# Kernel tuning notes

Hardware: AMD Instinct MI355X
Metric: run time of the kernel (lower is better)

Reference implementation:

```python
import jax, jax.numpy as jnp
import numpy as np

TEMP = 10.0
BPE = 4
BER = 0.01
K = 2 ** BPE  # number of centers


def setup_inputs() -> dict:
    key = jax.random.key(0)
    k1, k2 = jax.random.split(key)
    x = jax.random.normal(k1, (32, 256, 32, 32), dtype=jnp.float32)
    center = jax.random.normal(k2, (K,), dtype=jnp.float32)
    return {"x": x, "center": center}


def reference(x, center):
    # Q_type == 'Soft' path of quantizer_channel.forward
    # residuals to every center: [B, C, H, W, K]
    d = x[..., None] - center
    # nearest-center index (hard assignment)
    W_index = jnp.argmin(jnp.abs(d), axis=-1)  # int32 [B,C,H,W]
    # soft assignment and soft quantized value
    smx = jax.nn.softmax(-TEMP * (d * d), axis=-1)
    W_soft = jnp.einsum('bchwk,k->bchw', smx, center)
    # bitmap rows are the binary expansion of the index, MSB first;
    # map[W_index][..., j] == (W_index >> (BPE-1-j)) & 1
    shifts = jnp.arange(BPE - 1, -1, -1, dtype=jnp.int32)  # [BPE]
    bits = (W_index[..., None] >> shifts) & 1  # [B,C,H,W,BPE]
    # bernoulli bit-flip channel noise; (bit + noise) % 2 == XOR
    noise = jax.random.bernoulli(jax.random.key(42), BER, bits.shape).astype(bits.dtype)
    noisy_bits = bits ^ noise
    # index = sum_i 2^i * bits[..., BPE-1-i]  ==  dot with 2^shifts
    idx_noisy = jnp.sum(noisy_bits * (2 ** shifts), axis=-1)
    W_noisy = center[idx_noisy]
    # soft value with stop-gradient channel bias (straight-through noise)
    return W_soft + jax.lax.stop_gradient(W_noisy - W_soft)
```

## Files before the change

kernel.cpp:

```cpp
#include <hip/hip_runtime.h>
#include <stdint.h>


#define KS1 42u
#define KS2 0x1BD11BF0u
#define BERN_LT 42950144u

__device__ __forceinline__ uint32_t fkey(float f) {
  uint32_t u = __float_as_uint(f);
  return (u & 0x80000000u) ? ~u : (u | 0x80000000u);
}
__device__ __forceinline__ float finv(uint32_t k) {
  uint32_t u = (k & 0x80000000u) ? (k & 0x7fffffffu) : ~k;
  return __uint_as_float(u);
}

__global__ void quantizer_setup_kernel(const float* __restrict__ center,
                                       float* __restrict__ ws) {
  const int t = threadIdx.x;
  __shared__ float sval[16];
  __shared__ int   sidx[16];
  if (t < 16) {
    const float ct = center[t];
    int rank = 0;
    for (int j = 0; j < 16; ++j) {
      const float cj = center[j];
      rank += (cj < ct || (cj == ct && j < t)) ? 1 : 0;
    }
    sval[rank] = ct;
    sidx[rank] = t;
  }
  __syncthreads();
  if (t < 15) {
    const float sL = sval[t], sR = sval[t + 1];
    const bool tieLeft = sidx[t] < sidx[t + 1];
    uint32_t lo = fkey(sL), hi = fkey(sR);
    while (hi - lo > 1u) {
      const uint32_t mid = lo + ((hi - lo) >> 1);
      const float xm = finv(mid);
      const float dL = fabsf(xm - sL);
      const float dR = fabsf(xm - sR);
      const bool left = (dL < dR) || (dL == dR && tieLeft);
      if (left) lo = mid; else hi = mid;
    }
    ws[t] = finv(lo);
  }
  __syncthreads();
  if (t < 16) {
    ((uint32_t*)ws)[16 + t] = (uint32_t)sidx[t];
    if (t == 15) ((uint32_t*)ws)[15] = 0u;
  }
}

__device__ __forceinline__ uint32_t rotl(uint32_t x, int r) {
  return __builtin_amdgcn_alignbit(x, x, (32 - r) & 31);
}
#define TF_ROUND4(r)                                            \
  { _Pragma("unroll") for (int j = 0; j < 4; ++j) {             \
      y0[j] += y1[j];                                           \
      y1[j] = rotl(y1[j], (r)) ^ y0[j];                         \
  } }
#define TF_INJ4(a, b)                                           \
  { _Pragma("unroll") for (int j = 0; j < 4; ++j) {             \
      y0[j] += (a); y1[j] += (b);                               \
  } }

__global__ __launch_bounds__(256) void quantizer_channel_kernel(
    const float* __restrict__ x, const float* __restrict__ center,
    const float* __restrict__ ws, float* __restrict__ out, int n4)
{
  const int t = blockIdx.x * blockDim.x + threadIdx.x;
  if (t >= n4) return;

  const int lane   = threadIdx.x & 63;
  const int base_b = (lane & 48) << 2;

  const int ctab = __float_as_int(center[lane & 15]);
  const int stab = (int)((const uint32_t*)ws)[16 + (lane & 15)];

  const float4* wsf = (const float4*)ws;
  const float4 ta = wsf[0], tb = wsf[1], tc = wsf[2], td = wsf[3];
  const float T0 = ta.x, T1 = ta.y, T2  = ta.z, T3  = ta.w;
  const float T4 = tb.x, T5 = tb.y, T6  = tb.z, T7  = tb.w;
  const float T8 = tc.x, T9 = tc.y, T10 = tc.z, T11 = tc.w;
  const float T12 = td.x, T13 = td.y, T14 = td.z;

  const float4 xv = reinterpret_cast<const float4*>(x)[t];
  const float xe[4] = {xv.x, xv.y, xv.z, xv.w};
  float oe[4];
  const uint32_t cb = (uint32_t)t * 16u + KS1;

#pragma unroll
  for (int e = 0; e < 4; ++e) {
    uint32_t y0[4], y1[4];
    const uint32_t c0 = cb + 4u * (uint32_t)e;
#pragma unroll
    for (int j = 0; j < 4; ++j) { y0[j] = 0u; y1[j] = c0 + (uint32_t)j; }
    TF_ROUND4(13) TF_ROUND4(15) TF_ROUND4(26) TF_ROUND4(6)
    TF_INJ4(KS1, KS2 + 1u)
    TF_ROUND4(17) TF_ROUND4(29) TF_ROUND4(16) TF_ROUND4(24)
    TF_INJ4(KS2, 0u + 2u)
    TF_ROUND4(13) TF_ROUND4(15) TF_ROUND4(26) TF_ROUND4(6)
    TF_INJ4(0u, KS1 + 3u)
    TF_ROUND4(17) TF_ROUND4(29) TF_ROUND4(16) TF_ROUND4(24)
    TF_INJ4(KS1, KS2 + 4u)
    TF_ROUND4(13) TF_ROUND4(15) TF_ROUND4(26) TF_ROUND4(6)
    TF_INJ4(KS2, 0u + 5u)

    const uint32_t f =
        (((y0[0] ^ y1[0]) < BERN_LT) ? 8u : 0u) |
        (((y0[1] ^ y1[1]) < BERN_LT) ? 4u : 0u) |
        (((y0[2] ^ y1[2]) < BERN_LT) ? 2u : 0u) |
        (((y0[3] ^ y1[3]) < BERN_LT) ? 1u : 0u);

    const float v = xe[e];
    const bool b3_ = v > T7;
    const float s2 = b3_ ? T11 : T3;
    const bool b2_ = v > s2;
    const float s1 = b3_ ? (b2_ ? T13 : T9) : (b2_ ? T5 : T1);
    const bool b1_ = v > s1;
    const float u0 = b1_ ? T2  : T0;
    const float u1 = b1_ ? T6  : T4;
    const float u2 = b1_ ? T10 : T8;
    const float u3 = b1_ ? T14 : T12;
    const float s0 = b3_ ? (b2_ ? u3 : u2) : (b2_ ? u1 : u0);
    const bool b0_ = v > s0;
    const uint32_t cell = (b3_ ? 8u : 0u) | (b2_ ? 4u : 0u) |
                          (b1_ ? 2u : 0u) | (b0_ ? 1u : 0u);

    const int best = __builtin_amdgcn_ds_bpermute(base_b + (int)(cell << 2), stab);
    const int fin_addr = base_b + (int)((((uint32_t)best) ^ f) << 2);
    oe[e] = __int_as_float(__builtin_amdgcn_ds_bpermute(fin_addr, ctab));
  }

  float4 o4;
  o4.x = oe[0]; o4.y = oe[1]; o4.z = oe[2]; o4.w = oe[3];
  reinterpret_cast<float4*>(out)[t] = o4;
}

extern "C" void kernel_launch(void* const* d_in, const int* in_sizes, int n_in,
                              void* d_out, int out_size, void* d_ws, size_t ws_size,
                              hipStream_t stream)
{
  const float* x      = (const float*)d_in[0];
  const float* center = (const float*)d_in[1];
  float* out          = (float*)d_out;
  float* ws           = (float*)d_ws;

  hipLaunchKernelGGL(quantizer_setup_kernel, dim3(1), dim3(64), 0, stream,
                     center, ws);

  const int N  = in_sizes[0];
  const int n4 = N / 4;
  const int block = 256;
  const int grid  = (n4 + block - 1) / block;

  hipLaunchKernelGGL(quantizer_channel_kernel, dim3(grid), dim3(block), 0, stream,
                     x, center, ws, out, n4);
}
```

Baseline: 72.66 us.

## Split threefry noise generation into separate kernel with packed flip masks

Moves the Bernoulli noise generation (threefry hashing) into its own kernel, which writes one packed 16-bit flip mask per float4 into the workspace. A second kernel then does the centre lookup and the XOR using those stored masks. The intent is to separate the compute-heavy RNG from the memory-bound quantize pass so each kernel is simpler. In exchange it adds an extra kernel launch and extra global-memory traffic for writing and reading the masks. It falls back to the original fused kernel when the workspace is too small.

```diff
diff --git a/kernel.cpp b/kernel.cpp
--- a/kernel.cpp
+++ b/kernel.cpp
@@ -5,6 +5,7 @@
 #define KS1 42u
 #define KS2 0x1BD11BF0u
 #define BERN_LT 42950144u
+#define WS_FLIP_OFF 32
 
 __device__ __forceinline__ uint32_t fkey(float f) {
   uint32_t u = __float_as_uint(f);
@@ -64,10 +65,46 @@
   { _Pragma("unroll") for (int j = 0; j < 4; ++j) {             \
       y0[j] += (a); y1[j] += (b);                               \
   } }
-
-__global__ __launch_bounds__(256) void quantizer_channel_kernel(
+#define TF_BODY                                                 \
+  TF_ROUND4(13) TF_ROUND4(15) TF_ROUND4(26) TF_ROUND4(6)       \
+  TF_INJ4(KS1, KS2 + 1u)                                        \
+  TF_ROUND4(17) TF_ROUND4(29) TF_ROUND4(16) TF_ROUND4(24)      \
+  TF_INJ4(KS2, 0u + 2u)                                         \
+  TF_ROUND4(13) TF_ROUND4(15) TF_ROUND4(26) TF_ROUND4(6)       \
+  TF_INJ4(0u, KS1 + 3u)                                         \
+  TF_ROUND4(17) TF_ROUND4(29) TF_ROUND4(16) TF_ROUND4(24)      \
+  TF_INJ4(KS1, KS2 + 4u)                                        \
+  TF_ROUND4(13) TF_ROUND4(15) TF_ROUND4(26) TF_ROUND4(6)       \
+  TF_INJ4(KS2, 0u + 5u)
+
+__global__ __launch_bounds__(256) void noise_kernel(
+    uint16_t* __restrict__ flips, int n4)
+{
+  const int t = blockIdx.x * blockDim.x + threadIdx.x;
+  if (t >= n4) return;
+  const uint32_t cb = (uint32_t)t * 16u + KS1;
+  uint32_t packed = 0u;
+#pragma unroll
+  for (int e = 0; e < 4; ++e) {
+    uint32_t y0[4], y1[4];
+    const uint32_t c0 = cb + 4u * (uint32_t)e;
+#pragma unroll
+    for (int j = 0; j < 4; ++j) { y0[j] = 0u; y1[j] = c0 + (uint32_t)j; }
+    TF_BODY
+    const uint32_t nib =
+        (((y0[0] ^ y1[0]) < BERN_LT) ? 8u : 0u) |
+        (((y0[1] ^ y1[1]) < BERN_LT) ? 4u : 0u) |
+        (((y0[2] ^ y1[2]) < BERN_LT) ? 2u : 0u) |
+        (((y0[3] ^ y1[3]) < BERN_LT) ? 1u : 0u);
+    packed |= nib << (4 * e);
+  }
+  flips[t] = (uint16_t)packed;
+}
+
+__global__ __launch_bounds__(256) void finish_kernel(
     const float* __restrict__ x, const float* __restrict__ center,
-    const float* __restrict__ ws, float* __restrict__ out, int n4)
+    const float* __restrict__ ws, const uint16_t* __restrict__ flips,
+    float* __restrict__ out, int n4)
 {
   const int t = blockIdx.x * blockDim.x + threadIdx.x;
   if (t >= n4) return;
@@ -86,33 +123,12 @@
   const float T12 = td.x, T13 = td.y, T14 = td.z;
 
   const float4 xv = reinterpret_cast<const float4*>(x)[t];
+  const uint32_t fw = (uint32_t)flips[t];
   const float xe[4] = {xv.x, xv.y, xv.z, xv.w};
   float oe[4];
-  const uint32_t cb = (uint32_t)t * 16u + KS1;
 
 #pragma unroll
   for (int e = 0; e < 4; ++e) {
-    uint32_t y0[4], y1[4];
-    const uint32_t c0 = cb + 4u * (uint32_t)e;
-#pragma unroll
-    for (int j = 0; j < 4; ++j) { y0[j] = 0u; y1[j] = c0 + (uint32_t)j; }
-    TF_ROUND4(13) TF_ROUND4(15) TF_ROUND4(26) TF_ROUND4(6)
-    TF_INJ4(KS1, KS2 + 1u)
-    TF_ROUND4(17) TF_ROUND4(29) TF_ROUND4(16) TF_ROUND4(24)
-    TF_INJ4(KS2, 0u + 2u)
-    TF_ROUND4(13) TF_ROUND4(15) TF_ROUND4(26) TF_ROUND4(6)
-    TF_INJ4(0u, KS1 + 3u)
-    TF_ROUND4(17) TF_ROUND4(29) TF_ROUND4(16) TF_ROUND4(24)
-    TF_INJ4(KS1, KS2 + 4u)
-    TF_ROUND4(13) TF_ROUND4(15) TF_ROUND4(26) TF_ROUND4(6)
-    TF_INJ4(KS2, 0u + 5u)
-
-    const uint32_t f =
-        (((y0[0] ^ y1[0]) < BERN_LT) ? 8u : 0u) |
-        (((y0[1] ^ y1[1]) < BERN_LT) ? 4u : 0u) |
-        (((y0[2] ^ y1[2]) < BERN_LT) ? 2u : 0u) |
-        (((y0[3] ^ y1[3]) < BERN_LT) ? 1u : 0u);
-
     const float v = xe[e];
     const bool b3_ = v > T7;
     const float s2 = b3_ ? T11 : T3;
@@ -129,10 +145,66 @@
                           (b1_ ? 2u : 0u) | (b0_ ? 1u : 0u);
 
     const int best = __builtin_amdgcn_ds_bpermute(base_b + (int)(cell << 2), stab);
+    const uint32_t f = (fw >> (4 * e)) & 15u;
     const int fin_addr = base_b + (int)((((uint32_t)best) ^ f) << 2);
     oe[e] = __int_as_float(__builtin_amdgcn_ds_bpermute(fin_addr, ctab));
   }
 
+  float4 o4;
+  o4.x = oe[0]; o4.y = oe[1]; o4.z = oe[2]; o4.w = oe[3];
+  reinterpret_cast<float4*>(out)[t] = o4;
+}
+
+__global__ __launch_bounds__(256) void fused_kernel(
+    const float* __restrict__ x, const float* __restrict__ center,
+    const float* __restrict__ ws, float* __restrict__ out, int n4)
+{
+  const int t = blockIdx.x * blockDim.x + threadIdx.x;
+  if (t >= n4) return;
+  const int lane   = threadIdx.x & 63;
+  const int base_b = (lane & 48) << 2;
+  const int ctab = __float_as_int(center[lane & 15]);
+  const int stab = (int)((const uint32_t*)ws)[16 + (lane & 15)];
+  const float4* wsf = (const float4*)ws;
+  const float4 ta = wsf[0], tb = wsf[1], tc = wsf[2], td = wsf[3];
+  const float T0 = ta.x, T1 = ta.y, T2  = ta.z, T3  = ta.w;
+  const float T4 = tb.x, T5 = tb.y, T6  = tb.z, T7  = tb.w;
+  const float T8 = tc.x, T9 = tc.y, T10 = tc.z, T11 = tc.w;
+  const float T12 = td.x, T13 = td.y, T14 = td.z;
+  const float4 xv = reinterpret_cast<const float4*>(x)[t];
+  const float xe[4] = {xv.x, xv.y, xv.z, xv.w};
+  float oe[4];
+  const uint32_t cb = (uint32_t)t * 16u + KS1;
+#pragma unroll
+  for (int e = 0; e < 4; ++e) {
+    uint32_t y0[4], y1[4];
+    const uint32_t c0 = cb + 4u * (uint32_t)e;
+#pragma unroll
+    for (int j = 0; j < 4; ++j) { y0[j] = 0u; y1[j] = c0 + (uint32_t)j; }
+    TF_BODY
+    const uint32_t f =
+        (((y0[0] ^ y1[0]) < BERN_LT) ? 8u : 0u) |
+        (((y0[1] ^ y1[1]) < BERN_LT) ? 4u : 0u) |
+        (((y0[2] ^ y1[2]) < BERN_LT) ? 2u : 0u) |
+        (((y0[3] ^ y1[3]) < BERN_LT) ? 1u : 0u);
+    const float v = xe[e];
+    const bool b3_ = v > T7;
+    const float s2 = b3_ ? T11 : T3;
+    const bool b2_ = v > s2;
+    const float s1 = b3_ ? (b2_ ? T13 : T9) : (b2_ ? T5 : T1);
+    const bool b1_ = v > s1;
+    const float u0 = b1_ ? T2  : T0;
+    const float u1 = b1_ ? T6  : T4;
+    const float u2 = b1_ ? T10 : T8;
+    const float u3 = b1_ ? T14 : T12;
+    const float s0 = b3_ ? (b2_ ? u3 : u2) : (b2_ ? u1 : u0);
+    const bool b0_ = v > s0;
+    const uint32_t cell = (b3_ ? 8u : 0u) | (b2_ ? 4u : 0u) |
+                          (b1_ ? 2u : 0u) | (b0_ ? 1u : 0u);
+    const int best = __builtin_amdgcn_ds_bpermute(base_b + (int)(cell << 2), stab);
+    const int fin_addr = base_b + (int)((((uint32_t)best) ^ f) << 2);
+    oe[e] = __int_as_float(__builtin_amdgcn_ds_bpermute(fin_addr, ctab));
+  }
   float4 o4;
   o4.x = oe[0]; o4.y = oe[1]; o4.z = oe[2]; o4.w = oe[3];
   reinterpret_cast<float4*>(out)[t] = o4;
@@ -155,6 +227,15 @@
   const int block = 256;
   const int grid  = (n4 + block - 1) / block;
 
-  hipLaunchKernelGGL(quantizer_channel_kernel, dim3(grid), dim3(block), 0, stream,
-                     x, center, ws, out, n4);
-}
+  const size_t need = (size_t)WS_FLIP_OFF * 4 + (size_t)n4 * sizeof(uint16_t);
+  if (ws_size >= need) {
+    uint16_t* flips = (uint16_t*)((uint32_t*)ws + WS_FLIP_OFF);
+    hipLaunchKernelGGL(noise_kernel, dim3(grid), dim3(block), 0, stream,
+                       flips, n4);
+    hipLaunchKernelGGL(finish_kernel, dim3(grid), dim3(block), 0, stream,
+                       x, center, ws, flips, out, n4);
+  } else {
+    hipLaunchKernelGGL(fused_kernel, dim3(grid), dim3(block), 0, stream,
+                       x, center, ws, out, n4);
+  }
+}
```

Result: slower. 81.23 us (+11.8%).
